# Kernel tuning notes

Measured on AMD Instinct MI355X. Metric: run time of the kernel, lower is better.

The kernel has to match this reference:

```python
import jax, jax.numpy as jnp
import numpy as np

TEMPERATURE = 0.07
N_CLASSES = 100


def setup_inputs() -> dict:
    key = jax.random.key(0)
    k1, k2 = jax.random.split(key)
    N, D = 8192, 128
    emb = jax.random.normal(k1, (N, D), dtype=jnp.float32)
    # unit-normalize so exp(sim / temperature) stays finite in fp32
    emb = emb / jnp.linalg.norm(emb, axis=1, keepdims=True)
    labels = jax.random.randint(k2, (N,), 0, N_CLASSES, dtype=jnp.int64)
    return {"embeddings": emb, "labels": labels}


def reference(embeddings, labels):
    N = embeddings.shape[0]
    dt = embeddings.dtype
    # [N, N] similarity
    sim = jnp.matmul(embeddings, embeddings.T) / TEMPERATURE
    off_diag = 1.0 - jnp.eye(N, dtype=dt)
    pos_mask = (labels[:, None] == labels[None, :]).astype(dt) * off_diag
    exp_sim = jnp.exp(sim) * off_diag  # diagonal zeroed
    positive_sum = jnp.sum(exp_sim * pos_mask, axis=1)
    total_sum = jnp.sum(exp_sim, axis=1)
    loss = -jnp.log(positive_sum / (total_sum + 1e-8) + 1e-8)
    valid = pos_mask.sum(axis=1) > 0
    cnt = jnp.sum(valid.astype(dt))
    mean_loss = jnp.where(
        cnt > 0,
        jnp.sum(jnp.where(valid, loss, jnp.zeros_like(loss))) / jnp.maximum(cnt, 1.0),
        jnp.asarray(0.0, dtype=dt),
    )
    return mean_loss
```

## Files before the change

kernel.cpp:

```cpp
#include <hip/hip_runtime.h>

#define N 8192
#define D 128
#define SCALE_A 20.6098592f
#define NP 64
#define NBLK 512
#define NBLK_PREP 256

using short8  = __attribute__((ext_vector_type(8))) short;
using float4v = __attribute__((ext_vector_type(4))) float;

#if __has_builtin(__builtin_amdgcn_exp2f)
#define EXP2(x) __builtin_amdgcn_exp2f(x)
#else
#define EXP2(x) __expf((x) * 0.69314718f)
#endif

static __device__ inline unsigned int f2bf(float f) {
    union { float f; unsigned int u; } x;
    x.f = f;
    unsigned int u = x.u;
    return (u + 0x7FFFu + ((u >> 16) & 1u)) >> 16;
}

__global__ __launch_bounds__(256) void cl_prep(
    const float* __restrict__ emb, unsigned short* __restrict__ bfB,
    unsigned short* __restrict__ bfA, float* __restrict__ tot,
    int* __restrict__ ticket)
{
    const int t = blockIdx.x * 256 + threadIdx.x;
    const float* p = emb + (size_t)t * 16;
    uint4 ob[2], oa[2];
    #pragma unroll
    for (int h = 0; h < 2; ++h) {
        float4v f0 = *(const float4v*)(p + h * 8);
        float4v f1 = *(const float4v*)(p + h * 8 + 4);
        ob[h].x = f2bf(f0[0]) | (f2bf(f0[1]) << 16);
        ob[h].y = f2bf(f0[2]) | (f2bf(f0[3]) << 16);
        ob[h].z = f2bf(f1[0]) | (f2bf(f1[1]) << 16);
        ob[h].w = f2bf(f1[2]) | (f2bf(f1[3]) << 16);
        oa[h].x = f2bf(f0[0] * SCALE_A) | (f2bf(f0[1] * SCALE_A) << 16);
        oa[h].y = f2bf(f0[2] * SCALE_A) | (f2bf(f0[3] * SCALE_A) << 16);
        oa[h].z = f2bf(f1[0] * SCALE_A) | (f2bf(f1[1] * SCALE_A) << 16);
        oa[h].w = f2bf(f1[2] * SCALE_A) | (f2bf(f1[3] * SCALE_A) << 16);
    }
    ((uint4*)bfB)[t * 2]     = ob[0];
    ((uint4*)bfB)[t * 2 + 1] = ob[1];
    ((uint4*)bfA)[t * 2]     = oa[0];
    ((uint4*)bfA)[t * 2 + 1] = oa[1];
    if (t < 2 * N) tot[t] = 0.f;
    if (t == 0) *ticket = 0;
}

__global__ __launch_bounds__(512, 4) void cl_main(
    const unsigned short* __restrict__ bfA, const unsigned short* __restrict__ bfB,
    const int* __restrict__ labels,
    float* __restrict__ tot, float* __restrict__ pos,
    int* __restrict__ ticket, float* __restrict__ out)
{
    __shared__ uint4 ldsB[128 * 16];
    __shared__ float sred[2][8];
    __shared__ int   s_ticket;

    const int tid  = threadIdx.x;
    const int lane = tid & 63;
    const int wave = tid >> 6;
    const int q    = lane >> 4;
    const int c    = lane & 15;

    const int i   = blockIdx.x >> 3;
    const int cid = blockIdx.x & 7;
    const int nit = (cid == 0 && i < 32) ? 5 : 4;
    const int R0r = i * 128;
    const uint4* bfB4 = (const uint4*)bfB;

    int m0 = cid * 4;
    {
        const uint4* src = bfB4 + (size_t)(((i + m0) & 63) * 128) * 16;
        #pragma unroll
        for (int s = 0; s < 4; ++s) {
            const int g     = tid + s * 512;
            const int row   = g >> 4;
            const int chunk = g & 15;
            __builtin_amdgcn_global_load_lds(
                (const __attribute__((address_space(1))) void*)(src + row * 16 + (chunk ^ (row & 15))),
                (__attribute__((address_space(3))) void*)(&ldsB[g]),
                16, 0, 0);
        }
    }

    short8 afrag[4];
    int rowlab[4];
    {
        const int arow = R0r + wave * 16 + c;
        #pragma unroll
        for (int ks = 0; ks < 4; ++ks)
            afrag[ks] = *(const short8*)(bfA + (size_t)arow * D + ks * 32 + q * 8);
        #pragma unroll
        for (int reg = 0; reg < 4; ++reg)
            rowlab[reg] = labels[R0r + wave * 16 + q * 4 + reg];
    }
    int collab[8];
    #pragma unroll
    for (int tc = 0; tc < 8; ++tc)
        collab[tc] = labels[((i + m0) & 63) * 128 + tc * 16 + c];

    asm volatile("s_waitcnt vmcnt(0) lgkmcnt(0)" ::: "memory");
    __builtin_amdgcn_s_barrier();
    __builtin_amdgcn_sched_barrier(0);

    float tot_a[4] = {0.f, 0.f, 0.f, 0.f};
    float pos_a[4] = {0.f, 0.f, 0.f, 0.f};

    #pragma unroll 1
    for (int it = 0; it < nit; ++it) {
        const int m    = (cid == 0) ? ((it == 4) ? 32 : it) : (cid * 4 + it);
        const int j    = (i + m) & 63;
        const int C0   = j * 128;
        const bool diag = (m == 0);

        float4v acc[8];
        #pragma unroll
        for (int tc = 0; tc < 8; ++tc) {
            float4v z = {0.f, 0.f, 0.f, 0.f};
            acc[tc] = z;
        }
        const short8* ldsS = (const short8*)ldsB;
        #pragma unroll
        for (int ks = 0; ks < 4; ++ks) {
            const short8* pk = ldsS + c * 16 + ((ks * 4 + q) ^ c);
            #pragma unroll
            for (int tc = 0; tc < 8; ++tc) {
                if (diag && tc < wave) continue;
                short8 b = pk[tc * 256];
                acc[tc] = __builtin_amdgcn_mfma_f32_16x16x32_bf16(
                    afrag[ks], b, acc[tc], 0, 0, 0);
            }
        }

        float ctot[8] = {0,0,0,0,0,0,0,0};
        float cpos[8] = {0,0,0,0,0,0,0,0};
        #pragma unroll
        for (int tc = 0; tc < 8; ++tc) {
            if (diag && tc < wave) continue;
            const int lc = collab[tc];
            if (diag && tc == wave) {
                #pragma unroll
                for (int reg = 0; reg < 4; ++reg) {
                    float v = EXP2(acc[tc][reg]);
                    if ((q * 4 + reg) >= c) v = 0.f;
                    tot_a[reg] += v;  ctot[tc] += v;
                    if (rowlab[reg] == lc) { pos_a[reg] += v; cpos[tc] += v; }
                }
            } else {
                #pragma unroll
                for (int reg = 0; reg < 4; ++reg) {
                    float v = EXP2(acc[tc][reg]);
                    tot_a[reg] += v;  ctot[tc] += v;
                    if (rowlab[reg] == lc) { pos_a[reg] += v; cpos[tc] += v; }
                }
            }
        }

        #pragma unroll
        for (int tc = 0; tc < 8; ++tc) {
            if (diag && tc < wave) continue;
            float t = ctot[tc], p = cpos[tc];
            t += __shfl_xor(t, 16, 64);  t += __shfl_xor(t, 32, 64);
            p += __shfl_xor(p, 16, 64);  p += __shfl_xor(p, 32, 64);
            if (q == 0) {
                const int cc = C0 + tc * 16 + c;
                atomicAdd(&tot[cc], t);
                atomicAdd(&pos[cc], p);
            }
        }

        __builtin_amdgcn_sched_barrier(0);
        __builtin_amdgcn_s_barrier();
        __builtin_amdgcn_sched_barrier(0);

        if (it < nit - 1) {
            const int mn = (cid == 0) ? ((it + 1 == 4) ? 32 : it + 1)
                                      : (cid * 4 + it + 1);
            const int jn = (i + mn) & 63;
            const uint4* src = bfB4 + (size_t)(jn * 128) * 16;
            #pragma unroll
            for (int s = 0; s < 4; ++s) {
                const int g     = tid + s * 512;
                const int row   = g >> 4;
                const int chunk = g & 15;
                __builtin_amdgcn_global_load_lds(
                    (const __attribute__((address_space(1))) void*)(src + row * 16 + (chunk ^ (row & 15))),
                    (__attribute__((address_space(3))) void*)(&ldsB[g]),
                    16, 0, 0);
            }
            #pragma unroll
            for (int tc = 0; tc < 8; ++tc)
                collab[tc] = labels[jn * 128 + tc * 16 + c];
            asm volatile("s_waitcnt vmcnt(0)" ::: "memory");
            __builtin_amdgcn_s_barrier();
            __builtin_amdgcn_sched_barrier(0);
        }
    }

    #pragma unroll
    for (int reg = 0; reg < 4; ++reg) {
        float t = tot_a[reg];
        float p = pos_a[reg];
        #pragma unroll
        for (int m = 1; m < 16; m <<= 1) {
            t += __shfl_xor(t, m, 64);
            p += __shfl_xor(p, m, 64);
        }
        if (c == 0) {
            const int r = R0r + wave * 16 + q * 4 + reg;
            atomicAdd(&tot[r], t);
            atomicAdd(&pos[r], p);
        }
    }

    asm volatile("s_waitcnt vmcnt(0)" ::: "memory");
    __syncthreads();
    if (tid == 0)
        s_ticket = __hip_atomic_fetch_add(ticket, 1, __ATOMIC_RELAXED,
                                          __HIP_MEMORY_SCOPE_AGENT);
    __syncthreads();
    if (s_ticket != NBLK - 1) return;

    float lsum = 0.f, lcnt = 0.f;
    #pragma unroll 4
    for (int idx = tid; idx < N; idx += 512) {
        const float t = __hip_atomic_load(&tot[idx], __ATOMIC_RELAXED,
                                          __HIP_MEMORY_SCOPE_AGENT);
        const float p = __hip_atomic_load(&pos[idx], __ATOMIC_RELAXED,
                                          __HIP_MEMORY_SCOPE_AGENT);
        const float loss = -__logf(p / (t + 1e-8f) + 1e-8f);
        if (p > 0.f) { lsum += loss; lcnt += 1.f; }
    }
    #pragma unroll
    for (int m = 1; m < 64; m <<= 1) {
        lsum += __shfl_xor(lsum, m, 64);
        lcnt += __shfl_xor(lcnt, m, 64);
    }
    if (lane == 0) { sred[0][wave] = lsum; sred[1][wave] = lcnt; }
    __syncthreads();
    if (tid == 0) {
        float s = 0.f, n = 0.f;
        #pragma unroll
        for (int w = 0; w < 8; ++w) { s += sred[0][w]; n += sred[1][w]; }
        out[0] = (n > 0.f) ? s / fmaxf(n, 1.f) : 0.f;
    }
}

extern "C" void kernel_launch(void* const* d_in, const int* in_sizes, int n_in,
                              void* d_out, int out_size, void* d_ws, size_t ws_size,
                              hipStream_t stream) {
    const float* emb  = (const float*)d_in[0];
    const int* labels = (const int*)d_in[1];
    unsigned short* bfB = (unsigned short*)d_ws;
    unsigned short* bfA = bfB + (size_t)N * D;
    float* tot    = (float*)(bfA + (size_t)N * D);
    float* pos    = tot + N;
    int*   ticket = (int*)(pos + N);

    cl_prep<<<NBLK_PREP, 256, 0, stream>>>(emb, bfB, bfA, tot, ticket);
    cl_main<<<NBLK, 512, 0, stream>>>(bfA, bfB, labels, tot, pos,
                                      ticket, (float*)d_out);
}
```

Baseline: 97.27 us.

## Load B fragments directly from global memory instead of staging through LDS

The shared-memory staging of each 128-row B tile (global_load_lds with swizzle, plus block barriers) is removed. Each wave now reads its B operands straight from global memory into registers per MFMA, and column labels are loaded per iteration. This drops the LDS traffic and the two barriers per iteration. In exchange, the 8 waves each re-read the same tile from global/L2 (8x redundant traffic), the loads are no longer overlapped with compute, and launch bounds drop to 2 blocks per CU.

```diff
diff --git a/kernel.cpp b/kernel.cpp
--- a/kernel.cpp
+++ b/kernel.cpp
@@ -52,13 +52,12 @@
     if (t == 0) *ticket = 0;
 }
 
-__global__ __launch_bounds__(512, 4) void cl_main(
+__global__ __launch_bounds__(512, 2) void cl_main(
     const unsigned short* __restrict__ bfA, const unsigned short* __restrict__ bfB,
     const int* __restrict__ labels,
     float* __restrict__ tot, float* __restrict__ pos,
     int* __restrict__ ticket, float* __restrict__ out)
 {
-    __shared__ uint4 ldsB[128 * 16];
     __shared__ float sred[2][8];
     __shared__ int   s_ticket;
 
@@ -72,22 +71,6 @@
     const int cid = blockIdx.x & 7;
     const int nit = (cid == 0 && i < 32) ? 5 : 4;
     const int R0r = i * 128;
-    const uint4* bfB4 = (const uint4*)bfB;
-
-    int m0 = cid * 4;
-    {
-        const uint4* src = bfB4 + (size_t)(((i + m0) & 63) * 128) * 16;
-        #pragma unroll
-        for (int s = 0; s < 4; ++s) {
-            const int g     = tid + s * 512;
-            const int row   = g >> 4;
-            const int chunk = g & 15;
-            __builtin_amdgcn_global_load_lds(
-                (const __attribute__((address_space(1))) void*)(src + row * 16 + (chunk ^ (row & 15))),
-                (__attribute__((address_space(3))) void*)(&ldsB[g]),
-                16, 0, 0);
-        }
-    }
 
     short8 afrag[4];
     int rowlab[4];
@@ -100,14 +83,6 @@
         for (int reg = 0; reg < 4; ++reg)
             rowlab[reg] = labels[R0r + wave * 16 + q * 4 + reg];
     }
-    int collab[8];
-    #pragma unroll
-    for (int tc = 0; tc < 8; ++tc)
-        collab[tc] = labels[((i + m0) & 63) * 128 + tc * 16 + c];
-
-    asm volatile("s_waitcnt vmcnt(0) lgkmcnt(0)" ::: "memory");
-    __builtin_amdgcn_s_barrier();
-    __builtin_amdgcn_sched_barrier(0);
 
     float tot_a[4] = {0.f, 0.f, 0.f, 0.f};
     float pos_a[4] = {0.f, 0.f, 0.f, 0.f};
@@ -119,20 +94,24 @@
         const int C0   = j * 128;
         const bool diag = (m == 0);
 
+        int collab[8];
+        #pragma unroll
+        for (int tc = 0; tc < 8; ++tc)
+            collab[tc] = labels[C0 + tc * 16 + c];
+
         float4v acc[8];
         #pragma unroll
         for (int tc = 0; tc < 8; ++tc) {
             float4v z = {0.f, 0.f, 0.f, 0.f};
             acc[tc] = z;
         }
-        const short8* ldsS = (const short8*)ldsB;
-        #pragma unroll
-        for (int ks = 0; ks < 4; ++ks) {
-            const short8* pk = ldsS + c * 16 + ((ks * 4 + q) ^ c);
+        #pragma unroll
+        for (int tc = 0; tc < 8; ++tc) {
+            if (diag && tc < wave) continue;
+            const short8* bp = (const short8*)(bfB + (size_t)(C0 + tc * 16 + c) * D + q * 8);
             #pragma unroll
-            for (int tc = 0; tc < 8; ++tc) {
-                if (diag && tc < wave) continue;
-                short8 b = pk[tc * 256];
+            for (int ks = 0; ks < 4; ++ks) {
+                short8 b = bp[ks * 4];
                 acc[tc] = __builtin_amdgcn_mfma_f32_16x16x32_bf16(
                     afrag[ks], b, acc[tc], 0, 0, 0);
             }
@@ -174,33 +153,6 @@
                 atomicAdd(&pos[cc], p);
             }
         }
-
-        __builtin_amdgcn_sched_barrier(0);
-        __builtin_amdgcn_s_barrier();
-        __builtin_amdgcn_sched_barrier(0);
-
-        if (it < nit - 1) {
-            const int mn = (cid == 0) ? ((it + 1 == 4) ? 32 : it + 1)
-                                      : (cid * 4 + it + 1);
-            const int jn = (i + mn) & 63;
-            const uint4* src = bfB4 + (size_t)(jn * 128) * 16;
-            #pragma unroll
-            for (int s = 0; s < 4; ++s) {
-                const int g     = tid + s * 512;
-                const int row   = g >> 4;
-                const int chunk = g & 15;
-                __builtin_amdgcn_global_load_lds(
-                    (const __attribute__((address_space(1))) void*)(src + row * 16 + (chunk ^ (row & 15))),
-                    (__attribute__((address_space(3))) void*)(&ldsB[g]),
-                    16, 0, 0);
-            }
-            #pragma unroll
-            for (int tc = 0; tc < 8; ++tc)
-                collab[tc] = labels[jn * 128 + tc * 16 + c];
-            asm volatile("s_waitcnt vmcnt(0)" ::: "memory");
-            __builtin_amdgcn_s_barrier();
-            __builtin_amdgcn_sched_barrier(0);
-        }
     }
 
     #pragma unroll
```

Result: slower. 135.0 us (+38.8%).
